# Performance work log

Measured on AMD Instinct MI355X. Metric: run time of the kernel, lower is better.

Reference implementation:

```python
import jax, jax.numpy as jnp
import numpy as np

B, L, C = 32, 4096, 64
PL, PC = 64, 16          # patch sizes along L and C
NP = 256                 # num_patches
OUT = 512                # output_dim
FS = 1000.0              # sampling frequency -> T = 1/FS


def setup_inputs() -> dict:
    key = jax.random.key(0)
    ks = jax.random.split(key, 7)
    d_in = PL * (PC * 2)
    return {
        "x": jax.random.normal(ks[0], (B, L, C), dtype=jnp.float32),
        "start_L": jax.random.randint(ks[1], (B, NP), 0, L - PL + 1, dtype=jnp.int32),
        "start_C": jax.random.randint(ks[2], (B, NP), 0, C - PC + 1, dtype=jnp.int32),
        "w1": jax.random.normal(ks[3], (OUT, d_in), dtype=jnp.float32) / np.sqrt(d_in),
        "b1": jax.random.normal(ks[4], (OUT,), dtype=jnp.float32) * 0.01,
        "w2": jax.random.normal(ks[5], (OUT, OUT), dtype=jnp.float32) / np.sqrt(OUT),
        "b2": jax.random.normal(ks[6], (OUT,), dtype=jnp.float32) * 0.01,
    }


def reference(x, start_L, start_C, w1, b1, w2, b2):
    T = 1.0 / FS
    t = jnp.arange(L, dtype=jnp.float32) * T                      # [L]

    # patch index grids (wrapping, as in the torch module)
    idx_L = (start_L[:, :, None] + jnp.arange(PL, dtype=jnp.int32)) % L   # [B,NP,PL]
    idx_C = (start_C[:, :, None] + jnp.arange(PC, dtype=jnp.int32)) % C   # [B,NP,PC]

    # double gather: patches[b,p,i,j] = x[b, idx_L[b,p,i], idx_C[b,p,j]]
    b_idx = jnp.arange(B, dtype=jnp.int32)[:, None, None, None]
    patches = x[b_idx, idx_L[:, :, :, None], idx_C[:, :, None, :]]        # [B,NP,PL,PC]

    # time embedding gathered with the same L indices, broadcast over PC
    t_patches = jnp.broadcast_to(t[idx_L][:, :, :, None], (B, NP, PL, PC))

    feats = jnp.concatenate([patches, t_patches], axis=-1)                # [B,NP,PL,2*PC]
    feats = feats.reshape(B, NP, PL * 2 * PC)

    h = jnp.einsum('bpd,od->bpo', feats, w1) + b1
    h = jax.nn.silu(h)
    out = jnp.einsum('bpo,qo->bpq', h, w2) + b2                           # [B,NP,OUT]
    return out
```

## Files before the change

### kernel.cpp

```cpp
#include <hip/hip_runtime.h>
#include <hip/hip_bf16.h>
#include <stdint.h>

#define BB   32
#define LL   4096
#define CCH  64
#define PLh  64
#define PCh  16
#define NPp  256
#define DOUT 512
#define DINX 1024
#define MM   (BB * NPp)
#define TT   0.001f

using bf16 = __hip_bfloat16;
typedef __attribute__((ext_vector_type(8))) short bf16x8;
typedef __attribute__((ext_vector_type(4))) float f32x4;

__device__ __forceinline__ void async_copy16(void* lds, const void* g) {
    __builtin_amdgcn_global_load_lds(
        (const __attribute__((address_space(1))) void*)g,
        (__attribute__((address_space(3))) void*)lds,
        16, 0, 0);
}

__global__ __launch_bounds__(256) void convert_f32_bf16(
    const float* __restrict__ in, bf16* __restrict__ out, int n)
{
    int i = (blockIdx.x * 256 + threadIdx.x) * 4;
    if (i >= n) return;
    float4 v = *(const float4*)(in + i);
    union { bf16 h[4]; uint2 u; } p;
    p.h[0] = __float2bfloat16(v.x);
    p.h[1] = __float2bfloat16(v.y);
    p.h[2] = __float2bfloat16(v.z);
    p.h[3] = __float2bfloat16(v.w);
    *(uint2*)(out + i) = p.u;
}

__global__ __launch_bounds__(256) void convert_w1x(
    const float* __restrict__ w1, bf16* __restrict__ w1x)
{
    int i = (blockIdx.x * 256 + threadIdx.x) * 4;
    int o = i >> 10, r = i & 1023;
    int l = r >> 4, j = r & 15;
    float4 v = *(const float4*)(w1 + (size_t)o * 2048 + l * 32 + j);
    union { bf16 h[4]; uint2 u; } p;
    p.h[0] = __float2bfloat16(v.x);
    p.h[1] = __float2bfloat16(v.y);
    p.h[2] = __float2bfloat16(v.z);
    p.h[3] = __float2bfloat16(v.w);
    *(uint2*)(w1x + i) = p.u;
}

__global__ __launch_bounds__(64) void precompute_affine(
    const float* __restrict__ w1, const float* __restrict__ b1,
    float* __restrict__ A1, float* __restrict__ C1)
{
    const int o = blockIdx.x;
    const int l = threadIdx.x;
    const float* wr = w1 + (size_t)o * 2048 + l * 32 + 16;
    float s0 = 0.f;
#pragma unroll
    for (int j = 0; j < 16; ++j) s0 += wr[j];
    float s1 = (float)l * s0;
#pragma unroll
    for (int off = 32; off > 0; off >>= 1) {
        s0 += __shfl_down(s0, off);
        s1 += __shfl_down(s1, off);
    }
    if (l == 0) {
        A1[o] = TT * s0;
        C1[o] = b1[o] + TT * s1;
    }
}

__global__ __launch_bounds__(256) void gather_feats(
    const float* __restrict__ x, const int* __restrict__ startL,
    const int* __restrict__ startC, bf16* __restrict__ feats)
{
    const int m = blockIdx.x;
    const int b = m >> 8;
    const int t = threadIdx.x;
    const int l = t >> 2;
    const int j0 = (t & 3) * 4;
    const int sl = startL[m];
    const int sc = startC[m];
    const float* src = x + ((size_t)b * LL + (size_t)(sl + l)) * CCH + sc + j0;
    union { bf16 h[4]; uint2 u; } p;
#pragma unroll
    for (int i = 0; i < 4; ++i) p.h[i] = __float2bfloat16(src[i]);
    *(uint2*)(feats + (size_t)m * DINX + t * 4) = p.u;
}

template <bool FUSE1>
__global__ __launch_bounds__(256) void gemm_bt(
    const bf16* __restrict__ A,
    const bf16* __restrict__ Bt,
    const float* __restrict__ bias,
    const float* __restrict__ C1,
    const int*   __restrict__ sL,
    void* __restrict__ outp,
    const int N, const int K)
{
    constexpr int BK = 32;
    __shared__ __align__(16) bf16 As[64 * BK];
    __shared__ __align__(16) bf16 Bs[64 * BK];

    const int tid  = threadIdx.x;
    const int lane = tid & 63;
    const int wave = tid >> 6;
    const int row0 = blockIdx.x * 64;
    const int col0 = blockIdx.y * 64;

    const int  srow  = wave * 16 + (lane >> 2);
    const int  skoff = (lane & 3) * 8;
    const bf16* agp = A  + (size_t)(row0 + srow) * K + skoff;
    const bf16* bgp = Bt + (size_t)(col0 + srow) * K + skoff;
    bf16* as_dst = &As[wave * 16 * BK];
    bf16* bs_dst = &Bs[wave * 16 * BK];

    const int mw = (wave >> 1) * 32;
    const int nw = (wave & 1) * 32;
    const int fr = lane & 15;
    const int fq = lane >> 4;

    f32x4 acc[2][2] = {};

    for (int k0 = 0; k0 < K; k0 += BK) {
        __syncthreads();
        async_copy16(as_dst, agp + k0);
        async_copy16(bs_dst, bgp + k0);
        __syncthreads();

        bf16x8 af[2], bfm[2];
#pragma unroll
        for (int i = 0; i < 2; ++i)
            af[i] = *(const bf16x8*)&As[(mw + i * 16 + fr) * BK + fq * 8];
#pragma unroll
        for (int j = 0; j < 2; ++j)
            bfm[j] = *(const bf16x8*)&Bs[(nw + j * 16 + fr) * BK + fq * 8];
#pragma unroll
        for (int i = 0; i < 2; ++i)
#pragma unroll
            for (int j = 0; j < 2; ++j)
                acc[i][j] = __builtin_amdgcn_mfma_f32_16x16x32_bf16(
                    af[i], bfm[j], acc[i][j], 0, 0, 0);
    }

    float slr[2][4];
    if (FUSE1) {
#pragma unroll
        for (int i = 0; i < 2; ++i)
#pragma unroll
            for (int r = 0; r < 4; ++r)
                slr[i][r] = (float)sL[row0 + mw + i * 16 + fq * 4 + r];
    }

#pragma unroll
    for (int j = 0; j < 2; ++j) {
        const int col = col0 + nw + j * 16 + fr;
        const float bv = bias[col];
        const float cv = FUSE1 ? C1[col] : 0.f;
#pragma unroll
        for (int i = 0; i < 2; ++i) {
#pragma unroll
            for (int r = 0; r < 4; ++r) {
                const int row = row0 + mw + i * 16 + fq * 4 + r;
                float v;
                if (FUSE1) {
                    v = acc[i][j][r] + slr[i][r] * bv + cv;
                    v = v / (1.0f + __expf(-v));
                    ((bf16*)outp)[(size_t)row * N + col] = __float2bfloat16(v);
                } else {
                    v = acc[i][j][r] + bv;
                    ((float*)outp)[(size_t)row * N + col] = v;
                }
            }
        }
    }
}

extern "C" void kernel_launch(void* const* d_in, const int* in_sizes, int n_in,
                              void* d_out, int out_size, void* d_ws, size_t ws_size,
                              hipStream_t stream)
{
    const float* x  = (const float*)d_in[0];
    const int*   sL = (const int*)  d_in[1];
    const int*   sC = (const int*)  d_in[2];
    const float* w1 = (const float*)d_in[3];
    const float* b1 = (const float*)d_in[4];
    const float* w2 = (const float*)d_in[5];
    const float* b2 = (const float*)d_in[6];
    float* out = (float*)d_out;

    char* ws = (char*)d_ws;
    bf16* featsB = (bf16*)ws;
    size_t off = (size_t)MM * DINX * 2;
    bf16* w1xB = (bf16*)(ws + off); off += (size_t)DOUT * DINX * 2;
    bf16* w2B  = (bf16*)(ws + off); off += (size_t)DOUT * DOUT * 2;
    bf16* hB   = (bf16*)(ws + off); off += (size_t)MM * DOUT * 2;
    float* A1  = (float*)(ws + off); off += DOUT * 4;
    float* C1  = (float*)(ws + off);

    convert_w1x<<<(DOUT * DINX / 4 + 255) / 256, 256, 0, stream>>>(w1, w1xB);
    convert_f32_bf16<<<(DOUT * DOUT / 4 + 255) / 256, 256, 0, stream>>>(w2, w2B, DOUT * DOUT);
    precompute_affine<<<DOUT, 64, 0, stream>>>(w1, b1, A1, C1);
    gather_feats<<<MM, 256, 0, stream>>>(x, sL, sC, featsB);

    gemm_bt<true><<<dim3(MM / 64, DOUT / 64), 256, 0, stream>>>(
        featsB, w1xB, A1, C1, sL, hB, DOUT, DINX);

    gemm_bt<false><<<dim3(MM / 64, DOUT / 64), 256, 0, stream>>>(
        hB, w2B, b2, nullptr, nullptr, out, DOUT, DOUT);
}
```

Measured before the change: 133.7 us.

## Fuse patch gather into first GEMM, merge prep kernels, widen K tile

Removes the separate gather kernel and its bf16 feature buffer: the first GEMM now loads x patches straight from global memory, converts them to bf16 and writes them into padded LDS. The three weight-prep kernels are merged into one launch, and both GEMMs use BK=64 with launch bounds set for 4 blocks per SM. The gathered x rows are read again by each of the 8 column blocks instead of once, and the A-tile loads are synchronous rather than async LDS copies.

```diff
diff --git a/kernel.cpp b/kernel.cpp
--- a/kernel.cpp
+++ b/kernel.cpp
@@ -5,8 +5,6 @@
 #define BB   32
 #define LL   4096
 #define CCH  64
-#define PLh  64
-#define PCh  16
 #define NPp  256
 #define DOUT 512
 #define DINX 1024
@@ -24,87 +22,61 @@
         16, 0, 0);
 }
 
-__global__ __launch_bounds__(256) void convert_f32_bf16(
-    const float* __restrict__ in, bf16* __restrict__ out, int n)
-{
-    int i = (blockIdx.x * 256 + threadIdx.x) * 4;
-    if (i >= n) return;
-    float4 v = *(const float4*)(in + i);
+__device__ __forceinline__ uint2 pack4_bf16(float a, float b, float c, float d) {
     union { bf16 h[4]; uint2 u; } p;
-    p.h[0] = __float2bfloat16(v.x);
-    p.h[1] = __float2bfloat16(v.y);
-    p.h[2] = __float2bfloat16(v.z);
-    p.h[3] = __float2bfloat16(v.w);
-    *(uint2*)(out + i) = p.u;
-}
-
-__global__ __launch_bounds__(256) void convert_w1x(
-    const float* __restrict__ w1, bf16* __restrict__ w1x)
-{
-    int i = (blockIdx.x * 256 + threadIdx.x) * 4;
-    int o = i >> 10, r = i & 1023;
-    int l = r >> 4, j = r & 15;
-    float4 v = *(const float4*)(w1 + (size_t)o * 2048 + l * 32 + j);
-    union { bf16 h[4]; uint2 u; } p;
-    p.h[0] = __float2bfloat16(v.x);
-    p.h[1] = __float2bfloat16(v.y);
-    p.h[2] = __float2bfloat16(v.z);
-    p.h[3] = __float2bfloat16(v.w);
-    *(uint2*)(w1x + i) = p.u;
-}
-
-__global__ __launch_bounds__(64) void precompute_affine(
+    p.h[0] = __float2bfloat16(a);
+    p.h[1] = __float2bfloat16(b);
+    p.h[2] = __float2bfloat16(c);
+    p.h[3] = __float2bfloat16(d);
+    return p.u;
+}
+
+__global__ __launch_bounds__(256) void prep(
     const float* __restrict__ w1, const float* __restrict__ b1,
+    const float* __restrict__ w2,
+    bf16* __restrict__ w1x, bf16* __restrict__ w2b,
     float* __restrict__ A1, float* __restrict__ C1)
 {
-    const int o = blockIdx.x;
-    const int l = threadIdx.x;
-    const float* wr = w1 + (size_t)o * 2048 + l * 32 + 16;
-    float s0 = 0.f;
-#pragma unroll
-    for (int j = 0; j < 16; ++j) s0 += wr[j];
-    float s1 = (float)l * s0;
-#pragma unroll
-    for (int off = 32; off > 0; off >>= 1) {
-        s0 += __shfl_down(s0, off);
-        s1 += __shfl_down(s1, off);
-    }
-    if (l == 0) {
-        A1[o] = TT * s0;
-        C1[o] = b1[o] + TT * s1;
-    }
-}
-
-__global__ __launch_bounds__(256) void gather_feats(
-    const float* __restrict__ x, const int* __restrict__ startL,
-    const int* __restrict__ startC, bf16* __restrict__ feats)
-{
-    const int m = blockIdx.x;
-    const int b = m >> 8;
-    const int t = threadIdx.x;
-    const int l = t >> 2;
-    const int j0 = (t & 3) * 4;
-    const int sl = startL[m];
-    const int sc = startC[m];
-    const float* src = x + ((size_t)b * LL + (size_t)(sl + l)) * CCH + sc + j0;
-    union { bf16 h[4]; uint2 u; } p;
-#pragma unroll
-    for (int i = 0; i < 4; ++i) p.h[i] = __float2bfloat16(src[i]);
-    *(uint2*)(feats + (size_t)m * DINX + t * 4) = p.u;
-}
-
-template <bool FUSE1>
-__global__ __launch_bounds__(256) void gemm_bt(
-    const bf16* __restrict__ A,
-    const bf16* __restrict__ Bt,
-    const float* __restrict__ bias,
-    const float* __restrict__ C1,
-    const int*   __restrict__ sL,
-    void* __restrict__ outp,
-    const int N, const int K)
-{
-    constexpr int BK = 32;
-    __shared__ __align__(16) bf16 As[64 * BK];
+    const int blk = blockIdx.x;
+    if (blk < 512) {
+        int i = (blk * 256 + threadIdx.x) * 4;
+        int o = i >> 10, r = i & 1023;
+        int l = r >> 4, j = r & 15;
+        float4 v = *(const float4*)(w1 + (size_t)o * 2048 + l * 32 + j);
+        *(uint2*)(w1x + i) = pack4_bf16(v.x, v.y, v.z, v.w);
+    } else if (blk < 768) {
+        int i = ((blk - 512) * 256 + threadIdx.x) * 4;
+        float4 v = *(const float4*)(w2 + i);
+        *(uint2*)(w2b + i) = pack4_bf16(v.x, v.y, v.z, v.w);
+    } else {
+        const int o = (blk - 768) * 4 + (threadIdx.x >> 6);
+        const int l = threadIdx.x & 63;
+        const float* wr = w1 + (size_t)o * 2048 + l * 32 + 16;
+        float s0 = 0.f;
+#pragma unroll
+        for (int j = 0; j < 16; ++j) s0 += wr[j];
+        float s1 = (float)l * s0;
+#pragma unroll
+        for (int off = 32; off > 0; off >>= 1) {
+            s0 += __shfl_down(s0, off);
+            s1 += __shfl_down(s1, off);
+        }
+        if (l == 0) {
+            A1[o] = TT * s0;
+            C1[o] = b1[o] + TT * s1;
+        }
+    }
+}
+
+__global__ __launch_bounds__(256, 4) void gemm1_fused(
+    const float* __restrict__ x, const int* __restrict__ sL,
+    const int* __restrict__ sC, const bf16* __restrict__ w1x,
+    const float* __restrict__ A1, const float* __restrict__ C1,
+    bf16* __restrict__ h)
+{
+    constexpr int BK = 64;
+    constexpr int ASTR = 72;
+    __shared__ __align__(16) bf16 As[64 * ASTR];
     __shared__ __align__(16) bf16 Bs[64 * BK];
 
     const int tid  = threadIdx.x;
@@ -112,13 +84,20 @@
     const int wave = tid >> 6;
     const int row0 = blockIdx.x * 64;
     const int col0 = blockIdx.y * 64;
-
-    const int  srow  = wave * 16 + (lane >> 2);
-    const int  skoff = (lane & 3) * 8;
-    const bf16* agp = A  + (size_t)(row0 + srow) * K + skoff;
-    const bf16* bgp = Bt + (size_t)(col0 + srow) * K + skoff;
-    bf16* as_dst = &As[wave * 16 * BK];
-    bf16* bs_dst = &Bs[wave * 16 * BK];
+    const int b    = row0 >> 8;
+
+    const int grow = tid >> 2;
+    const int gseg = tid & 3;
+    const int gsl  = sL[row0 + grow];
+    const int gsc  = sC[row0 + grow];
+    const float* xb = x + (size_t)b * LL * CCH + gsc;
+    bf16* ad = &As[grow * ASTR + gseg * 16];
+
+    const int  brow  = wave * 16 + (lane >> 3);
+    const int  bkoff = (lane & 7) * 8;
+    const bf16* bgp = w1x + (size_t)(col0 + brow) * DINX + bkoff;
+    bf16* bs0 = &Bs[(wave * 16 + 0) * BK];
+    bf16* bs1 = &Bs[(wave * 16 + 8) * BK];
 
     const int mw = (wave >> 1) * 32;
     const int nw = (wave & 1) * 32;
@@ -127,57 +106,144 @@
 
     f32x4 acc[2][2] = {};
 
+    for (int k0 = 0, l0 = 0; k0 < DINX; k0 += BK, l0 += 4) {
+        const float* src = xb + (size_t)(gsl + l0 + gseg) * CCH;
+        float4 v0 = *(const float4*)(src);
+        float4 v1 = *(const float4*)(src + 4);
+        float4 v2 = *(const float4*)(src + 8);
+        float4 v3 = *(const float4*)(src + 12);
+
+        __syncthreads();
+        async_copy16(bs0, bgp + k0);
+        async_copy16(bs1, bgp + (size_t)8 * DINX + k0);
+        uint4 pk0, pk1;
+        uint2 a01 = pack4_bf16(v0.x, v0.y, v0.z, v0.w);
+        uint2 a23 = pack4_bf16(v1.x, v1.y, v1.z, v1.w);
+        pk0.x = a01.x; pk0.y = a01.y; pk0.z = a23.x; pk0.w = a23.y;
+        a01 = pack4_bf16(v2.x, v2.y, v2.z, v2.w);
+        a23 = pack4_bf16(v3.x, v3.y, v3.z, v3.w);
+        pk1.x = a01.x; pk1.y = a01.y; pk1.z = a23.x; pk1.w = a23.y;
+        *(uint4*)(ad)     = pk0;
+        *(uint4*)(ad + 8) = pk1;
+        __syncthreads();
+
+        bf16x8 af[2][2], bfr[2][2];
+#pragma unroll
+        for (int i = 0; i < 2; ++i)
+#pragma unroll
+            for (int ks = 0; ks < 2; ++ks)
+                af[i][ks] = *(const bf16x8*)&As[(mw + i * 16 + fr) * ASTR + ks * 32 + fq * 8];
+#pragma unroll
+        for (int j = 0; j < 2; ++j)
+#pragma unroll
+            for (int ks = 0; ks < 2; ++ks)
+                bfr[j][ks] = *(const bf16x8*)&Bs[(nw + j * 16 + fr) * BK + ks * 32 + fq * 8];
+#pragma unroll
+        for (int ks = 0; ks < 2; ++ks)
+#pragma unroll
+            for (int i = 0; i < 2; ++i)
+#pragma unroll
+                for (int j = 0; j < 2; ++j)
+                    acc[i][j] = __builtin_amdgcn_mfma_f32_16x16x32_bf16(
+                        af[i][ks], bfr[j][ks], acc[i][j], 0, 0, 0);
+    }
+
+    float slr[2][4];
+#pragma unroll
+    for (int i = 0; i < 2; ++i)
+#pragma unroll
+        for (int r = 0; r < 4; ++r)
+            slr[i][r] = (float)sL[row0 + mw + i * 16 + fq * 4 + r];
+#pragma unroll
+    for (int j = 0; j < 2; ++j) {
+        const int col = col0 + nw + j * 16 + fr;
+        const float av = A1[col];
+        const float cv = C1[col];
+#pragma unroll
+        for (int i = 0; i < 2; ++i)
+#pragma unroll
+            for (int r = 0; r < 4; ++r) {
+                const int row = row0 + mw + i * 16 + fq * 4 + r;
+                float v = acc[i][j][r] + slr[i][r] * av + cv;
+                v = v / (1.0f + __expf(-v));
+                h[(size_t)row * DOUT + col] = __float2bfloat16(v);
+            }
+    }
+}
+
+__global__ __launch_bounds__(256, 4) void gemm2(
+    const bf16* __restrict__ A,
+    const bf16* __restrict__ Bt,
+    const float* __restrict__ bias,
+    float* __restrict__ out)
+{
+    constexpr int BK = 64;
+    constexpr int K  = DOUT;
+    __shared__ __align__(16) bf16 As[64 * BK];
+    __shared__ __align__(16) bf16 Bs[64 * BK];
+
+    const int tid  = threadIdx.x;
+    const int lane = tid & 63;
+    const int wave = tid >> 6;
+    const int row0 = blockIdx.x * 64;
+    const int col0 = blockIdx.y * 64;
+
+    const int  srow  = wave * 16 + (lane >> 3);
+    const int  skoff = (lane & 7) * 8;
+    const bf16* agp = A  + (size_t)(row0 + srow) * K + skoff;
+    const bf16* bgp = Bt + (size_t)(col0 + srow) * K + skoff;
+    bf16* as0 = &As[(wave * 16 + 0) * BK];
+    bf16* as1 = &As[(wave * 16 + 8) * BK];
+    bf16* bs0 = &Bs[(wave * 16 + 0) * BK];
+    bf16* bs1 = &Bs[(wave * 16 + 8) * BK];
+
+    const int mw = (wave >> 1) * 32;
+    const int nw = (wave & 1) * 32;
+    const int fr = lane & 15;
+    const int fq = lane >> 4;
+
+    f32x4 acc[2][2] = {};
+
     for (int k0 = 0; k0 < K; k0 += BK) {
         __syncthreads();
-        async_copy16(as_dst, agp + k0);
-        async_copy16(bs_dst, bgp + k0);
-        __syncthreads();
-
-        bf16x8 af[2], bfm[2];
-#pragma unroll
-        for (int i = 0; i < 2; ++i)
-            af[i] = *(const bf16x8*)&As[(mw + i * 16 + fr) * BK + fq * 8];
+        async_copy16(as0, agp + k0);
+        async_copy16(as1, agp + (size_t)8 * K + k0);
+        async_copy16(bs0, bgp + k0);
+        async_copy16(bs1, bgp + (size_t)8 * K + k0);
+        __syncthreads();
+
+        bf16x8 af[2][2], bfr[2][2];
+#pragma unroll
+        for (int i = 0; i < 2; ++i)
+#pragma unroll
+            for (int ks = 0; ks < 2; ++ks)
+                af[i][ks] = *(const bf16x8*)&As[(mw + i * 16 + fr) * BK + ks * 32 + fq * 8];
 #pragma unroll
         for (int j = 0; j < 2; ++j)
-            bfm[j] = *(const bf16x8*)&Bs[(nw + j * 16 + fr) * BK + fq * 8];
-#pragma unroll
-        for (int i = 0; i < 2; ++i)
-#pragma unroll
-            for (int j = 0; j < 2; ++j)
-                acc[i][j] = __builtin_amdgcn_mfma_f32_16x16x32_bf16(
-                    af[i], bfm[j], acc[i][j], 0, 0, 0);
-    }
-
-    float slr[2][4];
-    if (FUSE1) {
-#pragma unroll
-        for (int i = 0; i < 2; ++i)
-#pragma unroll
-            for (int r = 0; r < 4; ++r)
-                slr[i][r] = (float)sL[row0 + mw + i * 16 + fq * 4 + r];
+#pragma unroll
+            for (int ks = 0; ks < 2; ++ks)
+                bfr[j][ks] = *(const bf16x8*)&Bs[(nw + j * 16 + fr) * BK + ks * 32 + fq * 8];
+#pragma unroll
+        for (int ks = 0; ks < 2; ++ks)
+#pragma unroll
+            for (int i = 0; i < 2; ++i)
+#pragma unroll
+                for (int j = 0; j < 2; ++j)
+                    acc[i][j] = __builtin_amdgcn_mfma_f32_16x16x32_bf16(
+                        af[i][ks], bfr[j][ks], acc[i][j], 0, 0, 0);
     }
 
 #pragma unroll
     for (int j = 0; j < 2; ++j) {
         const int col = col0 + nw + j * 16 + fr;
         const float bv = bias[col];
-        const float cv = FUSE1 ? C1[col] : 0.f;
-#pragma unroll
-        for (int i = 0; i < 2; ++i) {
+#pragma unroll
+        for (int i = 0; i < 2; ++i)
 #pragma unroll
             for (int r = 0; r < 4; ++r) {
                 const int row = row0 + mw + i * 16 + fq * 4 + r;
-                float v;
-                if (FUSE1) {
-                    v = acc[i][j][r] + slr[i][r] * bv + cv;
-                    v = v / (1.0f + __expf(-v));
-                    ((bf16*)outp)[(size_t)row * N + col] = __float2bfloat16(v);
-                } else {
-                    v = acc[i][j][r] + bv;
-                    ((float*)outp)[(size_t)row * N + col] = v;
-                }
+                out[(size_t)row * DOUT + col] = acc[i][j][r] + bv;
             }
-        }
     }
 }
 
@@ -195,22 +261,17 @@
     float* out = (float*)d_out;
 
     char* ws = (char*)d_ws;
-    bf16* featsB = (bf16*)ws;
-    size_t off = (size_t)MM * DINX * 2;
-    bf16* w1xB = (bf16*)(ws + off); off += (size_t)DOUT * DINX * 2;
-    bf16* w2B  = (bf16*)(ws + off); off += (size_t)DOUT * DOUT * 2;
-    bf16* hB   = (bf16*)(ws + off); off += (size_t)MM * DOUT * 2;
-    float* A1  = (float*)(ws + off); off += DOUT * 4;
-    float* C1  = (float*)(ws + off);
-
-    convert_w1x<<<(DOUT * DINX / 4 + 255) / 256, 256, 0, stream>>>(w1, w1xB);
-    convert_f32_bf16<<<(DOUT * DOUT / 4 + 255) / 256, 256, 0, stream>>>(w2, w2B, DOUT * DOUT);
-    precompute_affine<<<DOUT, 64, 0, stream>>>(w1, b1, A1, C1);
-    gather_feats<<<MM, 256, 0, stream>>>(x, sL, sC, featsB);
-
-    gemm_bt<true><<<dim3(MM / 64, DOUT / 64), 256, 0, stream>>>(
-        featsB, w1xB, A1, C1, sL, hB, DOUT, DINX);
-
-    gemm_bt<false><<<dim3(MM / 64, DOUT / 64), 256, 0, stream>>>(
-        hB, w2B, b2, nullptr, nullptr, out, DOUT, DOUT);
-}
+    bf16* w1x = (bf16*)ws;                         size_t off = (size_t)DOUT * DINX * 2;
+    bf16* w2b = (bf16*)(ws + off);                 off += (size_t)DOUT * DOUT * 2;
+    bf16* hB  = (bf16*)(ws + off);                 off += (size_t)MM * DOUT * 2;
+    float* A1 = (float*)(ws + off);                off += DOUT * 4;
+    float* C1 = (float*)(ws + off);
+
+    prep<<<896, 256, 0, stream>>>(w1, b1, w2, w1x, w2b, A1, C1);
+
+    gemm1_fused<<<dim3(MM / 64, DOUT / 64), 256, 0, stream>>>(
+        x, sL, sC, w1x, A1, C1, hB);
+
+    gemm2<<<dim3(MM / 64, DOUT / 64), 256, 0, stream>>>(
+        hB, w2b, b2, out);
+}
```

Result: slower. 148.8 us (+11.3%).
